# Performance work log

Measured on AMD Instinct MI355X. Metric: run time of the kernel, lower is better.

Reference implementation:

```python
import jax, jax.numpy as jnp
import numpy as np

B, T, U = 16, 300, 30
ENC_DIM = DEC_DIM = JOINER_DIM = 512
VOCAB = 500


def setup_inputs() -> dict:
    key = jax.random.key(0)
    ks = jax.random.split(key, 8)
    s_enc = 1.0 / np.sqrt(ENC_DIM)
    s_dec = 1.0 / np.sqrt(DEC_DIM)
    s_out = 1.0 / np.sqrt(JOINER_DIM)
    return {
        "encoder_out": jax.random.normal(ks[0], (B, T, ENC_DIM), jnp.float32),
        "decoder_out": jax.random.normal(ks[1], (B, U, DEC_DIM), jnp.float32),
        "W_enc": jax.random.uniform(ks[2], (JOINER_DIM, ENC_DIM), jnp.float32, -s_enc, s_enc),
        "b_enc": jax.random.uniform(ks[3], (JOINER_DIM,), jnp.float32, -s_enc, s_enc),
        "W_dec": jax.random.uniform(ks[4], (JOINER_DIM, DEC_DIM), jnp.float32, -s_dec, s_dec),
        "b_dec": jax.random.uniform(ks[5], (JOINER_DIM,), jnp.float32, -s_dec, s_dec),
        "W_out": jax.random.uniform(ks[6], (VOCAB, JOINER_DIM), jnp.float32, -s_out, s_out),
        "b_out": jax.random.uniform(ks[7], (VOCAB,), jnp.float32, -s_out, s_out),
    }


def reference(encoder_out, decoder_out, W_enc, b_enc, W_dec, b_dec, W_out, b_out):
    # Project encoder (B,T,J) and decoder (B,U,J)
    enc = jnp.einsum("btd,jd->btj", encoder_out, W_enc) + b_enc
    dec = jnp.einsum("bud,jd->buj", decoder_out, W_dec) + b_dec
    # Broadcast add -> (B,T,U,J), then vocab linear -> (B,T,U,V)
    joint = enc[:, :, None, :] + dec[:, None, :, :]
    logits = jnp.einsum("btuj,vj->btuv", joint, W_out) + b_out
    return logits
```

## Files before the change

kernel.cpp:

```cpp
#include <hip/hip_runtime.h>

constexpr int B_ = 16, T_ = 300, U_ = 30;
constexpr int J_ = 512;
constexpr int V_ = 500;
constexpr int BT_ = B_ * T_;
constexpr int BU_ = B_ * U_;
constexpr int KD  = 512;
constexpr int NP  = 512;

typedef __attribute__((ext_vector_type(8))) short short8v;
typedef __attribute__((ext_vector_type(4))) float f32x4;

__device__ __forceinline__ ushort f2bf(float f) {
    unsigned u = __builtin_bit_cast(unsigned, f);
    u += 0x7FFFu + ((u >> 16) & 1u);
    return (ushort)(u >> 16);
}

#define GLOAD16(gsrc, ldst)                                                   \
    __builtin_amdgcn_global_load_lds(                                         \
        (const __attribute__((address_space(1))) unsigned int*)(const void*)(gsrc), \
        (__attribute__((address_space(3))) unsigned int*)(void*)(ldst), 16, 0, 0)

__global__ __launch_bounds__(256) void prep(
    const float* __restrict__ enc, const float* __restrict__ dec,
    const float* __restrict__ W_enc, const float* __restrict__ W_dec,
    const float* __restrict__ W_out, const float* __restrict__ b_enc,
    const float* __restrict__ b_dec, const float* __restrict__ b_out,
    ushort* __restrict__ encB, ushort* __restrict__ decB,
    ushort* __restrict__ WeT, ushort* __restrict__ WdT,
    ushort* __restrict__ WoB, float* __restrict__ be, float* __restrict__ bd)
{
    __shared__ ushort ts[64][65];
    const int bid = blockIdx.x;
    const int tid = threadIdx.x;

    if (bid < 1200) {
        const size_t idx = (size_t)bid * 2048 + tid * 8;
        float4 f0 = *reinterpret_cast<const float4*>(enc + idx);
        float4 f1 = *reinterpret_cast<const float4*>(enc + idx + 4);
        short8v o; o[0]=(short)f2bf(f0.x); o[1]=(short)f2bf(f0.y);
        o[2]=(short)f2bf(f0.z); o[3]=(short)f2bf(f0.w);
        o[4]=(short)f2bf(f1.x); o[5]=(short)f2bf(f1.y);
        o[6]=(short)f2bf(f1.z); o[7]=(short)f2bf(f1.w);
        *reinterpret_cast<short8v*>(encB + idx) = o;
    } else if (bid < 1328) {
        const size_t idx = (size_t)(bid - 1200) * 2048 + tid * 8;
        const int row = (int)(idx >> 9);
        short8v o = {};
        if (row < BU_) {
            float4 f0 = *reinterpret_cast<const float4*>(dec + idx);
            float4 f1 = *reinterpret_cast<const float4*>(dec + idx + 4);
            o[0]=(short)f2bf(f0.x); o[1]=(short)f2bf(f0.y);
            o[2]=(short)f2bf(f0.z); o[3]=(short)f2bf(f0.w);
            o[4]=(short)f2bf(f1.x); o[5]=(short)f2bf(f1.y);
            o[6]=(short)f2bf(f1.z); o[7]=(short)f2bf(f1.w);
        }
        *reinterpret_cast<short8v*>(decB + idx) = o;
    } else if (bid < 1456) {
        const bool isE = bid < 1392;
        const int t = bid - (isE ? 1328 : 1392);
        const float*  W = isE ? W_enc : W_dec;
        ushort*      WT = isE ? WeT : WdT;
        const int r0 = (t >> 3) * 64, c0 = (t & 7) * 64;
        #pragma unroll
        for (int it = 0; it < 4; ++it) {
            const int idx = tid + it * 256;
            const int r = idx >> 4, c4 = (idx & 15) * 4;
            float4 f = *reinterpret_cast<const float4*>(&W[(size_t)(r0 + r) * 512 + c0 + c4]);
            ts[r][c4 + 0] = f2bf(f.x); ts[r][c4 + 1] = f2bf(f.y);
            ts[r][c4 + 2] = f2bf(f.z); ts[r][c4 + 3] = f2bf(f.w);
        }
        __syncthreads();
        #pragma unroll
        for (int it = 0; it < 4; ++it) {
            const int idx = tid + it * 256;
            const int c = idx >> 4, r4 = (idx & 15) * 4;
            ushort4 o;
            o.x = ts[r4 + 0][c]; o.y = ts[r4 + 1][c];
            o.z = ts[r4 + 2][c]; o.w = ts[r4 + 3][c];
            *reinterpret_cast<ushort4*>(&WT[(size_t)(c0 + c) * 512 + r0 + r4]) = o;
        }
    } else {
        const int v    = (bid - 1456) * 4 + (tid >> 6);
        const int lane = tid & 63;
        float4 f0 = make_float4(0, 0, 0, 0), f1 = f0;
        if (v < V_) {
            f0 = *reinterpret_cast<const float4*>(&W_out[(size_t)v * 512 + lane * 8]);
            f1 = *reinterpret_cast<const float4*>(&W_out[(size_t)v * 512 + lane * 8 + 4]);
        }
        short8v o; o[0]=(short)f2bf(f0.x); o[1]=(short)f2bf(f0.y);
        o[2]=(short)f2bf(f0.z); o[3]=(short)f2bf(f0.w);
        o[4]=(short)f2bf(f1.x); o[5]=(short)f2bf(f1.y);
        o[6]=(short)f2bf(f1.z); o[7]=(short)f2bf(f1.w);
        *reinterpret_cast<short8v*>(WoB + (size_t)v * 512 + lane * 8) = o;

        float4 e0 = *reinterpret_cast<const float4*>(b_enc + lane * 8);
        float4 e1 = *reinterpret_cast<const float4*>(b_enc + lane * 8 + 4);
        float4 d0 = *reinterpret_cast<const float4*>(b_dec + lane * 8);
        float4 d1 = *reinterpret_cast<const float4*>(b_dec + lane * 8 + 4);
        float sE = f0.x*e0.x + f0.y*e0.y + f0.z*e0.z + f0.w*e0.w
                 + f1.x*e1.x + f1.y*e1.y + f1.z*e1.z + f1.w*e1.w;
        float sD = f0.x*d0.x + f0.y*d0.y + f0.z*d0.z + f0.w*d0.w
                 + f1.x*d1.x + f1.y*d1.y + f1.z*d1.z + f1.w*d1.w;
        #pragma unroll
        for (int off = 32; off > 0; off >>= 1) {
            sE += __shfl_down(sE, off);
            sD += __shfl_down(sD, off);
        }
        if (lane == 0) {
            be[v] = (v < V_) ? sE : 0.0f;
            bd[v] = (v < V_) ? (sD + b_out[v]) : 0.0f;
        }
    }
}

template <bool OUT_BF16>
__device__ __forceinline__ void gemm_body(
    const ushort* __restrict__ A, const ushort* __restrict__ Bm,
    const float* __restrict__ bias, void* __restrict__ C,
    int m0, int n0)
{
    __shared__ ushort a_s[64 * 32];
    __shared__ ushort b_s[64 * 32];

    const int tid  = threadIdx.x;
    const int lane = tid & 63;
    const int wave = tid >> 6;
    const int wm   = wave >> 1, wn = wave & 1;

    const int srow = (wave << 4) + (lane >> 2);
    const int skc  = (lane & 3) * 8;
    ushort* a_dst = a_s + wave * 512;
    ushort* b_dst = b_s + wave * 512;

    const int r16 = lane & 15;
    const int kc  = lane >> 4;

    f32x4 acc[2][2] = {};

    for (int k0 = 0; k0 < KD; k0 += 32) {
        GLOAD16(A  + (size_t)(m0 + srow) * KD + k0 + skc, a_dst);
        GLOAD16(Bm + (size_t)(n0 + srow) * KD + k0 + skc, b_dst);
        __syncthreads();

        const short8v af0 = *reinterpret_cast<const short8v*>(&a_s[(wm*32 +      r16) * 32 + kc*8]);
        const short8v af1 = *reinterpret_cast<const short8v*>(&a_s[(wm*32 + 16 + r16) * 32 + kc*8]);
        const short8v bf0 = *reinterpret_cast<const short8v*>(&b_s[(wn*32 +      r16) * 32 + kc*8]);
        const short8v bf1 = *reinterpret_cast<const short8v*>(&b_s[(wn*32 + 16 + r16) * 32 + kc*8]);

        acc[0][0] = __builtin_amdgcn_mfma_f32_16x16x32_bf16(af0, bf0, acc[0][0], 0, 0, 0);
        acc[0][1] = __builtin_amdgcn_mfma_f32_16x16x32_bf16(af0, bf1, acc[0][1], 0, 0, 0);
        acc[1][0] = __builtin_amdgcn_mfma_f32_16x16x32_bf16(af1, bf0, acc[1][0], 0, 0, 0);
        acc[1][1] = __builtin_amdgcn_mfma_f32_16x16x32_bf16(af1, bf1, acc[1][1], 0, 0, 0);
        __syncthreads();
    }

    const int rb = (lane >> 4) * 4;
    #pragma unroll
    for (int m = 0; m < 2; ++m) {
        const int grow0 = m0 + wm * 32 + m * 16 + rb;
        #pragma unroll
        for (int n = 0; n < 2; ++n) {
            const int gcol = n0 + wn * 32 + n * 16 + r16;
            const float bv = bias ? bias[gcol] : 0.0f;
            #pragma unroll
            for (int r = 0; r < 4; ++r) {
                const float v = acc[m][n][r] + bv;
                if constexpr (OUT_BF16)
                    ((ushort*)C)[(size_t)(grow0 + r) * NP + gcol] = f2bf(v);
                else
                    ((float*)C)[(size_t)(grow0 + r) * NP + gcol] = v;
            }
        }
    }
}

__global__ __launch_bounds__(256) void wc_gemm(
    const ushort* __restrict__ WoB, const ushort* __restrict__ WeT,
    const ushort* __restrict__ WdT, ushort* __restrict__ WcE,
    ushort* __restrict__ WcD)
{
    const bool z = blockIdx.z != 0;
    gemm_body<true>(WoB, z ? WdT : WeT, nullptr, z ? WcD : WcE,
                    blockIdx.y * 64, blockIdx.x * 64);
}

__global__ __launch_bounds__(256) void evdv_gemm(
    const ushort* __restrict__ encB, const ushort* __restrict__ WcE,
    const float* __restrict__ be, float* __restrict__ EV,
    const ushort* __restrict__ decB, const ushort* __restrict__ WcD,
    const float* __restrict__ bd, float* __restrict__ DV)
{
    const bool z = blockIdx.z != 0;
    if (z && blockIdx.y >= 8) return;
    gemm_body<false>(z ? decB : encB, z ? WcD : WcE, z ? bd : be,
                     z ? DV : EV, blockIdx.y * 64, blockIdx.x * 64);
}

constexpr int V4 = V_ / 4;

__global__ __launch_bounds__(256) void bcast_add(
    const float* __restrict__ EV, const float* __restrict__ DV,
    float* __restrict__ out)
{
    __shared__ float evs[V_];
    const int bt = blockIdx.x;
    const int b  = bt / T_;

    const float4* evrow = reinterpret_cast<const float4*>(EV + (size_t)bt * NP);
    if (threadIdx.x < V4)
        reinterpret_cast<float4*>(evs)[threadIdx.x] = evrow[threadIdx.x];
    __syncthreads();

    const float* dvb  = DV + (size_t)b * U_ * NP;
    float4*      orow = reinterpret_cast<float4*>(out + (size_t)bt * U_ * V_);

    for (int i = threadIdx.x; i < U_ * V4; i += 256) {
        const int u = i / V4;
        const int v = i - u * V4;
        const float4 d = *reinterpret_cast<const float4*>(dvb + u * NP + v * 4);
        const float4 e = reinterpret_cast<const float4*>(evs)[v];
        float4 r;
        r.x = e.x + d.x; r.y = e.y + d.y; r.z = e.z + d.z; r.w = e.w + d.w;
        orow[i] = r;
    }
}

extern "C" void kernel_launch(void* const* d_in, const int* in_sizes, int n_in,
                              void* d_out, int out_size, void* d_ws, size_t ws_size,
                              hipStream_t stream) {
    const float* enc   = (const float*)d_in[0];
    const float* dec   = (const float*)d_in[1];
    const float* W_enc = (const float*)d_in[2];
    const float* b_enc = (const float*)d_in[3];
    const float* W_dec = (const float*)d_in[4];
    const float* b_dec = (const float*)d_in[5];
    const float* W_out = (const float*)d_in[6];
    const float* b_out = (const float*)d_in[7];
    float* out = (float*)d_out;

    char* p = (char*)d_ws;
    ushort* encB = (ushort*)p;            p += (size_t)BT_ * 512 * 2;
    ushort* decB = (ushort*)p;            p += (size_t)512 * 512 * 2;
    ushort* WeT  = (ushort*)p;            p += (size_t)512 * 512 * 2;
    ushort* WdT  = (ushort*)p;            p += (size_t)512 * 512 * 2;
    ushort* WoB  = (ushort*)p;            p += (size_t)512 * 512 * 2;
    ushort* WcE  = (ushort*)p;            p += (size_t)512 * 512 * 2;
    ushort* WcD  = (ushort*)p;            p += (size_t)512 * 512 * 2;
    float*  be   = (float*)p;             p += 512 * 4;
    float*  bd   = (float*)p;             p += 512 * 4;
    float*  EV   = (float*)p;             p += (size_t)BT_ * 512 * 4;
    float*  DV   = (float*)p;

    dim3 blk(256);

    prep<<<dim3(1584), blk, 0, stream>>>(
        enc, dec, W_enc, W_dec, W_out, b_enc, b_dec, b_out,
        encB, decB, WeT, WdT, WoB, be, bd);

    wc_gemm<<<dim3(8, 8, 2), blk, 0, stream>>>(WoB, WeT, WdT, WcE, WcD);

    evdv_gemm<<<dim3(8, BT_ / 64, 2), blk, 0, stream>>>(
        encB, WcE, be, EV, decB, WcD, bd, DV);

    bcast_add<<<dim3(BT_), blk, 0, stream>>>(EV, DV, out);
}
```

Before: 83.64 us.

## Double-buffer GEMM K-loop with 64-wide stages and streamline broadcast-add with nontemporal stores

The shared GEMM body now stages 64-wide K slices into double-buffered LDS. The next slice's global-to-LDS loads are issued before computing on the current one, which halves the barrier count and overlaps load latency with MFMA work. The broadcast-add kernel gets a fixed 2D thread mapping (tx over vocab quads, ty over U) in place of per-element division, and writes the large output with nontemporal stores so it does not pollute cache. LDS use per block rises fourfold, which may reduce occupancy.

After: 104.2 us. 24.6% more time.

```diff
diff --git a/kernel.cpp b/kernel.cpp
--- a/kernel.cpp
+++ b/kernel.cpp
@@ -121,8 +121,8 @@
     const float* __restrict__ bias, void* __restrict__ C,
     int m0, int n0)
 {
-    __shared__ ushort a_s[64 * 32];
-    __shared__ ushort b_s[64 * 32];
+    __shared__ ushort a_s[2][2][64 * 32];
+    __shared__ ushort b_s[2][2][64 * 32];
 
     const int tid  = threadIdx.x;
     const int lane = tid & 63;
@@ -131,30 +131,45 @@
 
     const int srow = (wave << 4) + (lane >> 2);
     const int skc  = (lane & 3) * 8;
-    ushort* a_dst = a_s + wave * 512;
-    ushort* b_dst = b_s + wave * 512;
+    const ushort* aptr = A  + (size_t)(m0 + srow) * KD + skc;
+    const ushort* bptr = Bm + (size_t)(n0 + srow) * KD + skc;
+    const int ldst = wave * 512;
 
     const int r16 = lane & 15;
     const int kc  = lane >> 4;
 
     f32x4 acc[2][2] = {};
 
-    for (int k0 = 0; k0 < KD; k0 += 32) {
-        GLOAD16(A  + (size_t)(m0 + srow) * KD + k0 + skc, a_dst);
-        GLOAD16(Bm + (size_t)(n0 + srow) * KD + k0 + skc, b_dst);
+    auto STAGE = [&](int buf, int k0) {
+        GLOAD16(aptr + k0,      &a_s[buf][0][ldst]);
+        GLOAD16(aptr + k0 + 32, &a_s[buf][1][ldst]);
+        GLOAD16(bptr + k0,      &b_s[buf][0][ldst]);
+        GLOAD16(bptr + k0 + 32, &b_s[buf][1][ldst]);
+    };
+    auto COMPUTE = [&](int buf) {
+        #pragma unroll
+        for (int ks = 0; ks < 2; ++ks) {
+            const short8v af0 = *reinterpret_cast<const short8v*>(&a_s[buf][ks][(wm*32 +      r16)*32 + kc*8]);
+            const short8v af1 = *reinterpret_cast<const short8v*>(&a_s[buf][ks][(wm*32 + 16 + r16)*32 + kc*8]);
+            const short8v bf0 = *reinterpret_cast<const short8v*>(&b_s[buf][ks][(wn*32 +      r16)*32 + kc*8]);
+            const short8v bf1 = *reinterpret_cast<const short8v*>(&b_s[buf][ks][(wn*32 + 16 + r16)*32 + kc*8]);
+            acc[0][0] = __builtin_amdgcn_mfma_f32_16x16x32_bf16(af0, bf0, acc[0][0], 0, 0, 0);
+            acc[0][1] = __builtin_amdgcn_mfma_f32_16x16x32_bf16(af0, bf1, acc[0][1], 0, 0, 0);
+            acc[1][0] = __builtin_amdgcn_mfma_f32_16x16x32_bf16(af1, bf0, acc[1][0], 0, 0, 0);
+            acc[1][1] = __builtin_amdgcn_mfma_f32_16x16x32_bf16(af1, bf1, acc[1][1], 0, 0, 0);
+        }
+    };
+
+    STAGE(0, 0);
+    __syncthreads();
+    #pragma unroll
+    for (int t = 0; t < 7; ++t) {
+        const int cur = t & 1;
+        STAGE(cur ^ 1, (t + 1) * 64);
+        COMPUTE(cur);
         __syncthreads();
-
-        const short8v af0 = *reinterpret_cast<const short8v*>(&a_s[(wm*32 +      r16) * 32 + kc*8]);
-        const short8v af1 = *reinterpret_cast<const short8v*>(&a_s[(wm*32 + 16 + r16) * 32 + kc*8]);
-        const short8v bf0 = *reinterpret_cast<const short8v*>(&b_s[(wn*32 +      r16) * 32 + kc*8]);
-        const short8v bf1 = *reinterpret_cast<const short8v*>(&b_s[(wn*32 + 16 + r16) * 32 + kc*8]);
-
-        acc[0][0] = __builtin_amdgcn_mfma_f32_16x16x32_bf16(af0, bf0, acc[0][0], 0, 0, 0);
-        acc[0][1] = __builtin_amdgcn_mfma_f32_16x16x32_bf16(af0, bf1, acc[0][1], 0, 0, 0);
-        acc[1][0] = __builtin_amdgcn_mfma_f32_16x16x32_bf16(af1, bf0, acc[1][0], 0, 0, 0);
-        acc[1][1] = __builtin_amdgcn_mfma_f32_16x16x32_bf16(af1, bf1, acc[1][1], 0, 0, 0);
-        __syncthreads();
-    }
+    }
+    COMPUTE(1);
 
     const int rb = (lane >> 4) * 4;
     #pragma unroll
@@ -198,32 +213,33 @@
                      z ? DV : EV, blockIdx.y * 64, blockIdx.x * 64);
 }
 
-constexpr int V4 = V_ / 4;
-
 __global__ __launch_bounds__(256) void bcast_add(
     const float* __restrict__ EV, const float* __restrict__ DV,
     float* __restrict__ out)
 {
-    __shared__ float evs[V_];
+    __shared__ f32x4 evs[128];
     const int bt = blockIdx.x;
     const int b  = bt / T_;
-
-    const float4* evrow = reinterpret_cast<const float4*>(EV + (size_t)bt * NP);
-    if (threadIdx.x < V4)
-        reinterpret_cast<float4*>(evs)[threadIdx.x] = evrow[threadIdx.x];
+    const int tx = threadIdx.x & 127;
+    const int ty = threadIdx.x >> 7;
+
+    if (threadIdx.x < 125) {
+        const f32x4* evrow = reinterpret_cast<const f32x4*>(EV + (size_t)bt * NP);
+        evs[threadIdx.x] = __builtin_nontemporal_load(evrow + threadIdx.x);
+    }
     __syncthreads();
 
-    const float* dvb  = DV + (size_t)b * U_ * NP;
-    float4*      orow = reinterpret_cast<float4*>(out + (size_t)bt * U_ * V_);
-
-    for (int i = threadIdx.x; i < U_ * V4; i += 256) {
-        const int u = i / V4;
-        const int v = i - u * V4;
-        const float4 d = *reinterpret_cast<const float4*>(dvb + u * NP + v * 4);
-        const float4 e = reinterpret_cast<const float4*>(evs)[v];
-        float4 r;
-        r.x = e.x + d.x; r.y = e.y + d.y; r.z = e.z + d.z; r.w = e.w + d.w;
-        orow[i] = r;
+    const bool active = tx < 125;
+    const f32x4 e = active ? evs[tx] : (f32x4){0, 0, 0, 0};
+    const float* dvb  = DV + (size_t)b * U_ * NP + tx * 4;
+    f32x4*       orow = reinterpret_cast<f32x4*>(out + (size_t)bt * U_ * 500) + tx;
+
+    if (active) {
+        #pragma unroll 3
+        for (int u = ty; u < U_; u += 2) {
+            const f32x4 d = *reinterpret_cast<const f32x4*>(dvb + u * NP);
+            __builtin_nontemporal_store(e + d, orow + u * 125);
+        }
     }
 }
 
```

## Fuse encoder-vocab GEMM with broadcast add, drop EV round-trip

Applied to the files above, without the earlier changes.

The encoder-side projection GEMM is merged into the broadcast-add kernel. Each 64x64 tile keeps its EV result in LDS and writes the (row, u, v) output slab directly, instead of storing EV to global memory and reading it back in a separate kernel. The decoder GEMM becomes its own small kernel that runs first. This removes the EV write and read and one kernel launch. The cost is less parallelism in the output-write phase (600 blocks instead of 4800), and every block now does its GEMM before it can start the large output store.

Result: slower. 92.37 us (+10.4%).

```diff
diff --git a/kernel.cpp b/kernel.cpp
--- a/kernel.cpp
+++ b/kernel.cpp
@@ -186,44 +186,101 @@
                     blockIdx.y * 64, blockIdx.x * 64);
 }
 
-__global__ __launch_bounds__(256) void evdv_gemm(
-    const ushort* __restrict__ encB, const ushort* __restrict__ WcE,
-    const float* __restrict__ be, float* __restrict__ EV,
+__global__ __launch_bounds__(256) void dv_gemm(
     const ushort* __restrict__ decB, const ushort* __restrict__ WcD,
     const float* __restrict__ bd, float* __restrict__ DV)
 {
-    const bool z = blockIdx.z != 0;
-    if (z && blockIdx.y >= 8) return;
-    gemm_body<false>(z ? decB : encB, z ? WcD : WcE, z ? bd : be,
-                     z ? DV : EV, blockIdx.y * 64, blockIdx.x * 64);
-}
-
-constexpr int V4 = V_ / 4;
-
-__global__ __launch_bounds__(256) void bcast_add(
-    const float* __restrict__ EV, const float* __restrict__ DV,
+    gemm_body<false>(decB, WcD, bd, DV, blockIdx.y * 64, blockIdx.x * 64);
+}
+
+__global__ __launch_bounds__(256) void fused_ev_bcast(
+    const ushort* __restrict__ encB, const ushort* __restrict__ WcE,
+    const float* __restrict__ be, const float* __restrict__ DV,
     float* __restrict__ out)
 {
-    __shared__ float evs[V_];
-    const int bt = blockIdx.x;
-    const int b  = bt / T_;
-
-    const float4* evrow = reinterpret_cast<const float4*>(EV + (size_t)bt * NP);
-    if (threadIdx.x < V4)
-        reinterpret_cast<float4*>(evs)[threadIdx.x] = evrow[threadIdx.x];
+    __shared__ ushort a_s[64 * 32];
+    __shared__ ushort b_s[64 * 32];
+    __shared__ float  evs[64 * 72];
+    __shared__ float  dvs[2 * 30 * 72];
+
+    const int tid  = threadIdx.x;
+    const int lane = tid & 63;
+    const int wave = tid >> 6;
+    const int wm   = wave >> 1, wn = wave & 1;
+    const int m0   = blockIdx.y * 64;
+    const int n0   = blockIdx.x * 64;
+
+    const int srow = (wave << 4) + (lane >> 2);
+    const int skc  = (lane & 3) * 8;
+    ushort* a_dst = a_s + wave * 512;
+    ushort* b_dst = b_s + wave * 512;
+
+    const int r16 = lane & 15;
+    const int kc  = lane >> 4;
+
+    f32x4 acc[2][2] = {};
+
+    for (int k0 = 0; k0 < KD; k0 += 32) {
+        GLOAD16(encB + (size_t)(m0 + srow) * KD + k0 + skc, a_dst);
+        GLOAD16(WcE  + (size_t)(n0 + srow) * KD + k0 + skc, b_dst);
+        __syncthreads();
+
+        const short8v af0 = *reinterpret_cast<const short8v*>(&a_s[(wm*32 +      r16) * 32 + kc*8]);
+        const short8v af1 = *reinterpret_cast<const short8v*>(&a_s[(wm*32 + 16 + r16) * 32 + kc*8]);
+        const short8v bf0 = *reinterpret_cast<const short8v*>(&b_s[(wn*32 +      r16) * 32 + kc*8]);
+        const short8v bf1 = *reinterpret_cast<const short8v*>(&b_s[(wn*32 + 16 + r16) * 32 + kc*8]);
+
+        acc[0][0] = __builtin_amdgcn_mfma_f32_16x16x32_bf16(af0, bf0, acc[0][0], 0, 0, 0);
+        acc[0][1] = __builtin_amdgcn_mfma_f32_16x16x32_bf16(af0, bf1, acc[0][1], 0, 0, 0);
+        acc[1][0] = __builtin_amdgcn_mfma_f32_16x16x32_bf16(af1, bf0, acc[1][0], 0, 0, 0);
+        acc[1][1] = __builtin_amdgcn_mfma_f32_16x16x32_bf16(af1, bf1, acc[1][1], 0, 0, 0);
+        __syncthreads();
+    }
+
+    const int rb = (lane >> 4) * 4;
+    #pragma unroll
+    for (int n = 0; n < 2; ++n) {
+        const int col = wn * 32 + n * 16 + r16;
+        const float bv = be[n0 + col];
+        #pragma unroll
+        for (int m = 0; m < 2; ++m) {
+            const int row = wm * 32 + m * 16 + rb;
+            #pragma unroll
+            for (int r = 0; r < 4; ++r)
+                evs[(row + r) * 72 + col] = acc[m][n][r] + bv;
+        }
+    }
+
+    const int b0 = m0 / T_;
+    const int b1 = (m0 + 63) / T_;
+    for (int i = tid; i < 960; i += 256) {
+        const int s   = i / 480;
+        const int rem = i - s * 480;
+        const int u   = rem >> 4;
+        const int v4  = rem & 15;
+        const int bb  = s ? b1 : b0;
+        const f32x4 d = *reinterpret_cast<const f32x4*>(
+            DV + ((size_t)bb * U_ + u) * NP + n0 + 4 * v4);
+        *reinterpret_cast<f32x4*>(&dvs[(s * U_ + u) * 72 + 4 * v4]) = d;
+    }
     __syncthreads();
 
-    const float* dvb  = DV + (size_t)b * U_ * NP;
-    float4*      orow = reinterpret_cast<float4*>(out + (size_t)bt * U_ * V_);
-
-    for (int i = threadIdx.x; i < U_ * V4; i += 256) {
-        const int u = i / V4;
-        const int v = i - u * V4;
-        const float4 d = *reinterpret_cast<const float4*>(dvb + u * NP + v * 4);
-        const float4 e = reinterpret_cast<const float4*>(evs)[v];
-        float4 r;
-        r.x = e.x + d.x; r.y = e.y + d.y; r.z = e.z + d.z; r.w = e.w + d.w;
-        orow[i] = r;
+    const int v4  = tid & 15;
+    const int nv4 = (n0 == 448) ? 13 : 16;
+    if (v4 < nv4) {
+        const int rsplit = (b0 + 1) * T_ - m0;
+        int u = tid >> 4;
+        int row = 0;
+        #pragma unroll 4
+        for (int it = 0; it < 120; ++it) {
+            const f32x4 e = *reinterpret_cast<const f32x4*>(&evs[row * 72 + 4 * v4]);
+            const int bsel = (row >= rsplit) ? 1 : 0;
+            const f32x4 d = *reinterpret_cast<const f32x4*>(&dvs[(bsel * U_ + u) * 72 + 4 * v4]);
+            float* o = out + ((size_t)(m0 + row) * U_ + u) * V_ + n0 + 4 * v4;
+            *reinterpret_cast<f32x4*>(o) = e + d;
+            u += 16;
+            if (u >= U_) { u -= U_; ++row; }
+        }
     }
 }
 
@@ -250,7 +307,6 @@
     ushort* WcD  = (ushort*)p;            p += (size_t)512 * 512 * 2;
     float*  be   = (float*)p;             p += 512 * 4;
     float*  bd   = (float*)p;             p += 512 * 4;
-    float*  EV   = (float*)p;             p += (size_t)BT_ * 512 * 4;
     float*  DV   = (float*)p;
 
     dim3 blk(256);
@@ -261,8 +317,8 @@
 
     wc_gemm<<<dim3(8, 8, 2), blk, 0, stream>>>(WoB, WeT, WdT, WcE, WcD);
 
-    evdv_gemm<<<dim3(8, BT_ / 64, 2), blk, 0, stream>>>(
-        encB, WcE, be, EV, decB, WcD, bd, DV);
-
-    bcast_add<<<dim3(BT_), blk, 0, stream>>>(EV, DV, out);
-}
+    dv_gemm<<<dim3(8, 8), blk, 0, stream>>>(decB, WcD, bd, DV);
+
+    fused_ev_bcast<<<dim3(8, BT_ / 64), blk, 0, stream>>>(
+        encB, WcE, be, DV, out);
+}
```

## Fuse encoder GEMM with broadcast-add output stream, drop encB/EV intermediates

Applied to the files above, without the earlier changes.

The encoder bf16 conversion, the encoder-by-WcE GEMM and the broadcast add are merged into one kernel. Each block converts a 32-row encoder tile into LDS, runs MFMA against WcE read directly from global memory, stages the EV rows in LDS, and streams the output with nontemporal stores. Each thread keeps its DV values in registers. This removes the encB and EV round trips through global memory and one launch. In exchange only 160 blocks are launched, and the B operand is loaded from global without LDS staging, which may limit occupancy and GEMM efficiency.

Result: slower. 111.0 us (+32.7%).

```diff
diff --git a/kernel.cpp b/kernel.cpp
--- a/kernel.cpp
+++ b/kernel.cpp
@@ -1,7 +1,6 @@
 #include <hip/hip_runtime.h>
 
 constexpr int B_ = 16, T_ = 300, U_ = 30;
-constexpr int J_ = 512;
 constexpr int V_ = 500;
 constexpr int BT_ = B_ * T_;
 constexpr int BU_ = B_ * U_;
@@ -22,12 +21,12 @@
         (const __attribute__((address_space(1))) unsigned int*)(const void*)(gsrc), \
         (__attribute__((address_space(3))) unsigned int*)(void*)(ldst), 16, 0, 0)
 
-__global__ __launch_bounds__(256) void prep(
-    const float* __restrict__ enc, const float* __restrict__ dec,
+__global__ __launch_bounds__(256) void prep2(
+    const float* __restrict__ dec,
     const float* __restrict__ W_enc, const float* __restrict__ W_dec,
     const float* __restrict__ W_out, const float* __restrict__ b_enc,
     const float* __restrict__ b_dec, const float* __restrict__ b_out,
-    ushort* __restrict__ encB, ushort* __restrict__ decB,
+    ushort* __restrict__ decB,
     ushort* __restrict__ WeT, ushort* __restrict__ WdT,
     ushort* __restrict__ WoB, float* __restrict__ be, float* __restrict__ bd)
 {
@@ -35,17 +34,8 @@
     const int bid = blockIdx.x;
     const int tid = threadIdx.x;
 
-    if (bid < 1200) {
+    if (bid < 128) {
         const size_t idx = (size_t)bid * 2048 + tid * 8;
-        float4 f0 = *reinterpret_cast<const float4*>(enc + idx);
-        float4 f1 = *reinterpret_cast<const float4*>(enc + idx + 4);
-        short8v o; o[0]=(short)f2bf(f0.x); o[1]=(short)f2bf(f0.y);
-        o[2]=(short)f2bf(f0.z); o[3]=(short)f2bf(f0.w);
-        o[4]=(short)f2bf(f1.x); o[5]=(short)f2bf(f1.y);
-        o[6]=(short)f2bf(f1.z); o[7]=(short)f2bf(f1.w);
-        *reinterpret_cast<short8v*>(encB + idx) = o;
-    } else if (bid < 1328) {
-        const size_t idx = (size_t)(bid - 1200) * 2048 + tid * 8;
         const int row = (int)(idx >> 9);
         short8v o = {};
         if (row < BU_) {
@@ -57,9 +47,9 @@
             o[6]=(short)f2bf(f1.z); o[7]=(short)f2bf(f1.w);
         }
         *reinterpret_cast<short8v*>(decB + idx) = o;
-    } else if (bid < 1456) {
-        const bool isE = bid < 1392;
-        const int t = bid - (isE ? 1328 : 1392);
+    } else if (bid < 256) {
+        const bool isE = bid < 192;
+        const int t = bid - (isE ? 128 : 192);
         const float*  W = isE ? W_enc : W_dec;
         ushort*      WT = isE ? WeT : WdT;
         const int r0 = (t >> 3) * 64, c0 = (t & 7) * 64;
@@ -82,7 +72,7 @@
             *reinterpret_cast<ushort4*>(&WT[(size_t)(c0 + c) * 512 + r0 + r4]) = o;
         }
     } else {
-        const int v    = (bid - 1456) * 4 + (tid >> 6);
+        const int v    = (bid - 256) * 4 + (tid >> 6);
         const int lane = tid & 63;
         float4 f0 = make_float4(0, 0, 0, 0), f1 = f0;
         if (v < V_) {
@@ -129,10 +119,10 @@
     const int wave = tid >> 6;
     const int wm   = wave >> 1, wn = wave & 1;
 
+    ushort* a_dst = a_s + wave * 512;
+    ushort* b_dst = b_s + wave * 512;
     const int srow = (wave << 4) + (lane >> 2);
     const int skc  = (lane & 3) * 8;
-    ushort* a_dst = a_s + wave * 512;
-    ushort* b_dst = b_s + wave * 512;
 
     const int r16 = lane & 15;
     const int kc  = lane >> 4;
@@ -186,44 +176,117 @@
                     blockIdx.y * 64, blockIdx.x * 64);
 }
 
-__global__ __launch_bounds__(256) void evdv_gemm(
-    const ushort* __restrict__ encB, const ushort* __restrict__ WcE,
-    const float* __restrict__ be, float* __restrict__ EV,
+__global__ __launch_bounds__(256) void dv_gemm(
     const ushort* __restrict__ decB, const ushort* __restrict__ WcD,
     const float* __restrict__ bd, float* __restrict__ DV)
 {
-    const bool z = blockIdx.z != 0;
-    if (z && blockIdx.y >= 8) return;
-    gemm_body<false>(z ? decB : encB, z ? WcD : WcE, z ? bd : be,
-                     z ? DV : EV, blockIdx.y * 64, blockIdx.x * 64);
-}
-
-constexpr int V4 = V_ / 4;
-
-__global__ __launch_bounds__(256) void bcast_add(
-    const float* __restrict__ EV, const float* __restrict__ DV,
+    gemm_body<false>(decB, WcD, bd, DV, blockIdx.y * 64, blockIdx.x * 64);
+}
+
+__global__ __launch_bounds__(512) void fused_ev_stream(
+    const float* __restrict__ enc, const ushort* __restrict__ WcE,
+    const float* __restrict__ be, const float* __restrict__ DV,
     float* __restrict__ out)
 {
-    __shared__ float evs[V_];
-    const int bt = blockIdx.x;
-    const int b  = bt / T_;
-
-    const float4* evrow = reinterpret_cast<const float4*>(EV + (size_t)bt * NP);
-    if (threadIdx.x < V4)
-        reinterpret_cast<float4*>(evs)[threadIdx.x] = evrow[threadIdx.x];
+    __shared__ __align__(16) char ls[64000];
+    ushort* a_s = reinterpret_cast<ushort*>(ls);
+    float*  evs = reinterpret_cast<float*>(ls);
+
+    const int tid  = threadIdx.x;
+    const int lane = tid & 63;
+    const int wave = tid >> 6;
+    const int b    = blockIdx.x / 10;
+    const int tile = blockIdx.x - b * 10;
+    const int t0   = tile * 32;
+    const int bt0  = b * T_ + t0;
+    const int rows = (tile < 9) ? 32 : 12;
+
+    const int ug   = tid >> 7;
+    const int v4   = tid & 127;
+    const bool vact = v4 < 125;
+    const int ucnt = (ug < 3) ? 8 : 6;
+    f32x4 dreg[8] = {};
+    if (vact) {
+        #pragma unroll
+        for (int j = 0; j < 8; ++j) {
+            const int u = ug * 8 + j;
+            if (u < U_)
+                dreg[j] = *reinterpret_cast<const f32x4*>(
+                    DV + ((size_t)b * U_ + u) * NP + v4 * 4);
+        }
+    }
+
+    #pragma unroll
+    for (int pass = 0; pass < 2; ++pass) {
+        const int u16 = tid + pass * 512;
+        const int r   = u16 >> 5;
+        const int c16 = (u16 & 31) * 16;
+        const int rr  = (r < rows) ? r : (rows - 1);
+        const float* src = enc + (size_t)(bt0 + rr) * 512 + c16;
+        float4 f0 = *reinterpret_cast<const float4*>(src);
+        float4 f1 = *reinterpret_cast<const float4*>(src + 4);
+        float4 f2 = *reinterpret_cast<const float4*>(src + 8);
+        float4 f3 = *reinterpret_cast<const float4*>(src + 12);
+        short8v o0, o1;
+        o0[0]=(short)f2bf(f0.x); o0[1]=(short)f2bf(f0.y);
+        o0[2]=(short)f2bf(f0.z); o0[3]=(short)f2bf(f0.w);
+        o0[4]=(short)f2bf(f1.x); o0[5]=(short)f2bf(f1.y);
+        o0[6]=(short)f2bf(f1.z); o0[7]=(short)f2bf(f1.w);
+        o1[0]=(short)f2bf(f2.x); o1[1]=(short)f2bf(f2.y);
+        o1[2]=(short)f2bf(f2.z); o1[3]=(short)f2bf(f2.w);
+        o1[4]=(short)f2bf(f3.x); o1[5]=(short)f2bf(f3.y);
+        o1[6]=(short)f2bf(f3.z); o1[7]=(short)f2bf(f3.w);
+        *reinterpret_cast<short8v*>(&a_s[r * 520 + c16])     = o0;
+        *reinterpret_cast<short8v*>(&a_s[r * 520 + c16 + 8]) = o1;
+    }
     __syncthreads();
 
-    const float* dvb  = DV + (size_t)b * U_ * NP;
-    float4*      orow = reinterpret_cast<float4*>(out + (size_t)bt * U_ * V_);
-
-    for (int i = threadIdx.x; i < U_ * V4; i += 256) {
-        const int u = i / V4;
-        const int v = i - u * V4;
-        const float4 d = *reinterpret_cast<const float4*>(dvb + u * NP + v * 4);
-        const float4 e = reinterpret_cast<const float4*>(evs)[v];
-        float4 r;
-        r.x = e.x + d.x; r.y = e.y + d.y; r.z = e.z + d.z; r.w = e.w + d.w;
-        orow[i] = r;
+    const int r16 = lane & 15;
+    const int kc8 = (lane >> 4) * 8;
+    const int cb  = wave * 64;
+    f32x4 acc[2][4] = {};
+
+    #pragma unroll 4
+    for (int k0 = 0; k0 < KD; k0 += 32) {
+        const short8v a0 = *reinterpret_cast<const short8v*>(&a_s[(r16)      * 520 + k0 + kc8]);
+        const short8v a1 = *reinterpret_cast<const short8v*>(&a_s[(16 + r16) * 520 + k0 + kc8]);
+        #pragma unroll
+        for (int n = 0; n < 4; ++n) {
+            const short8v bf = *reinterpret_cast<const short8v*>(
+                WcE + (size_t)(cb + n * 16 + r16) * KD + k0 + kc8);
+            acc[0][n] = __builtin_amdgcn_mfma_f32_16x16x32_bf16(a0, bf, acc[0][n], 0, 0, 0);
+            acc[1][n] = __builtin_amdgcn_mfma_f32_16x16x32_bf16(a1, bf, acc[1][n], 0, 0, 0);
+        }
+    }
+    __syncthreads();
+
+    const int rb = (lane >> 4) * 4;
+    #pragma unroll
+    for (int n = 0; n < 4; ++n) {
+        const int col = cb + n * 16 + r16;
+        if (col < V_) {
+            const float bv = be[col];
+            #pragma unroll
+            for (int m = 0; m < 2; ++m)
+                #pragma unroll
+                for (int r = 0; r < 4; ++r)
+                    evs[(m * 16 + rb + r) * V_ + col] = acc[m][n][r] + bv;
+        }
+    }
+    __syncthreads();
+
+    if (vact) {
+        float* ob = out + ((size_t)bt0 * U_ + ug * 8) * V_ + v4 * 4;
+        for (int r = 0; r < rows; ++r) {
+            const f32x4 e = *reinterpret_cast<const f32x4*>(&evs[r * V_ + v4 * 4]);
+            float* orow = ob + (size_t)r * U_ * V_;
+            #pragma unroll
+            for (int j = 0; j < 8; ++j) {
+                if (j < ucnt)
+                    __builtin_nontemporal_store(
+                        e + dreg[j], reinterpret_cast<f32x4*>(orow + j * V_));
+            }
+        }
     }
 }
 
@@ -241,7 +304,6 @@
     float* out = (float*)d_out;
 
     char* p = (char*)d_ws;
-    ushort* encB = (ushort*)p;            p += (size_t)BT_ * 512 * 2;
     ushort* decB = (ushort*)p;            p += (size_t)512 * 512 * 2;
     ushort* WeT  = (ushort*)p;            p += (size_t)512 * 512 * 2;
     ushort* WdT  = (ushort*)p;            p += (size_t)512 * 512 * 2;
@@ -250,19 +312,16 @@
     ushort* WcD  = (ushort*)p;            p += (size_t)512 * 512 * 2;
     float*  be   = (float*)p;             p += 512 * 4;
     float*  bd   = (float*)p;             p += 512 * 4;
-    float*  EV   = (float*)p;             p += (size_t)BT_ * 512 * 4;
     float*  DV   = (float*)p;
 
-    dim3 blk(256);
-
-    prep<<<dim3(1584), blk, 0, stream>>>(
-        enc, dec, W_enc, W_dec, W_out, b_enc, b_dec, b_out,
-        encB, decB, WeT, WdT, WoB, be, bd);
-
-    wc_gemm<<<dim3(8, 8, 2), blk, 0, stream>>>(WoB, WeT, WdT, WcE, WcD);
-
-    evdv_gemm<<<dim3(8, BT_ / 64, 2), blk, 0, stream>>>(
-        encB, WcE, be, EV, decB, WcD, bd, DV);
-
-    bcast_add<<<dim3(BT_), blk, 0, stream>>>(EV, DV, out);
-}
+    prep2<<<dim3(384), dim3(256), 0, stream>>>(
+        dec, W_enc, W_dec, W_out, b_enc, b_dec, b_out,
+        decB, WeT, WdT, WoB, be, bd);
+
+    wc_gemm<<<dim3(8, 8, 2), dim3(256), 0, stream>>>(WoB, WeT, WdT, WcE, WcD);
+
+    dv_gemm<<<dim3(8, 8), dim3(256), 0, stream>>>(decB, WcD, bd, DV);
+
+    fused_ev_stream<<<dim3(160), dim3(512), 0, stream>>>(
+        enc, WcE, be, DV, out);
+}
```
